# Optimization experiments

Hardware: AMD Instinct MI355X
Metric: run time of the kernel (lower is better)

The kernel has to match this reference:

```python
import jax, jax.numpy as jnp
import numpy as np

N_NODES = 100000
N_EDGES = 1600000
IN_FEATS = 128
HIDDEN = 128
NUM_CLASSES = 64


def setup_inputs() -> dict:
    key = jax.random.key(0)
    k1, k2, k3, k4, k5 = jax.random.split(key, 5)
    inputs = jax.random.normal(k1, (N_NODES, IN_FEATS), dtype=jnp.float32)
    src = jax.random.randint(k2, (N_EDGES,), 0, N_NODES, dtype=jnp.int32)
    dst = jax.random.randint(k3, (N_EDGES,), 0, N_NODES, dtype=jnp.int32)
    W1 = jax.random.normal(k4, (IN_FEATS, HIDDEN), dtype=jnp.float32) / np.sqrt(IN_FEATS)
    b1 = jnp.zeros((HIDDEN,), dtype=jnp.float32)
    W2 = jax.random.normal(k5, (HIDDEN, NUM_CLASSES), dtype=jnp.float32) / np.sqrt(HIDDEN)
    b2 = jnp.zeros((NUM_CLASSES,), dtype=jnp.float32)
    return {"inputs": inputs, "src": src, "dst": dst, "W1": W1, "b1": b1, "W2": W2, "b2": b2}


def _graph_conv(x, src, dst, W, b, n_nodes):
    # DGL GraphConv, norm='both': h = D_in^{-1/2} A D_out^{-1/2} x W + b
    ones = jnp.ones(src.shape[0], dtype=x.dtype)
    deg_out = jax.ops.segment_sum(ones, src, num_segments=n_nodes)
    deg_in = jax.ops.segment_sum(ones, dst, num_segments=n_nodes)
    norm_src = jax.lax.rsqrt(jnp.clip(deg_out, 1.0))  # [N]
    norm_dst = jax.lax.rsqrt(jnp.clip(deg_in, 1.0))   # [N]
    x = x * norm_src[:, None]
    msgs = x[src]                                      # [E, d] gather
    agg = jax.ops.segment_sum(msgs, dst, num_segments=n_nodes)  # [N, d] scatter-add
    agg = agg * norm_dst[:, None]
    return agg @ W + b


def reference(inputs, src, dst, W1, b1, W2, b2):
    n = inputs.shape[0]
    h = _graph_conv(inputs, src, dst, W1, b1, n)
    h = jax.nn.relu(h)
    h = _graph_conv(h, src, dst, W2, b2, n)
    return h
```

## Files before the change

### kernel.cpp

```cpp
#include <hip/hip_runtime.h>
#include <hip/hip_bf16.h>

#define N_FEATS_IN 128
#define BK_BITS 8
#define BK_SIZE 256
#define EPB 4096
#define MAXNB 512

typedef _Float16 h8 __attribute__((ext_vector_type(8)));
typedef float    f4v __attribute__((ext_vector_type(4)));
typedef float    f8v __attribute__((ext_vector_type(8)));

__device__ inline int wave_incl_scan(int v) {
    const int lane = threadIdx.x & 63;
    for (int off = 1; off < 64; off <<= 1) {
        int u = __shfl_up(v, off, 64);
        if (lane >= off) v += u;
    }
    return v;
}

__device__ inline int block_excl_scan(int s, int* ws, int* total) {
    const int lane = threadIdx.x & 63, wid = threadIdx.x >> 6;
    int inc = wave_incl_scan(s);
    if (lane == 63) ws[wid] = inc;
    __syncthreads();
    int woff = 0;
#pragma unroll
    for (int w = 0; w < 4; ++w) woff += (w < wid) ? ws[w] : 0;
    if (total) *total = ws[0] + ws[1] + ws[2] + ws[3];
    return woff + inc - s;
}

__global__ __launch_bounds__(256) void hist_kernel(
    const int* __restrict__ src, const int* __restrict__ dst,
    int* __restrict__ bh_d, int* __restrict__ bh_s,
    const float* __restrict__ W1, const float* __restrict__ W2,
    _Float16* __restrict__ wf1g, _Float16* __restrict__ wf2g,
    int E, int NB) {
    __shared__ int hd[MAXNB];
    __shared__ int hs[MAXNB];
    const int t = threadIdx.x;

    const int widx = blockIdx.x * 256 + t;
    if (widx < 128 * 128) {
        const int i = widx;
        const int k = i >> 7, c = i & 127;
        const int tt = c >> 4, s = k >> 5, q = (k >> 3) & 3, j = k & 7;
        wf1g[(((tt * 4 + s) * 4 + q) * 16 + (c & 15)) * 8 + j] =
            (_Float16)W1[i];
    } else if (widx < 128 * 128 + 128 * 64) {
        const int i = widx - 128 * 128;
        const int k = i >> 6, c = i & 63;
        const int tt = c >> 4, s = k >> 5, q = (k >> 3) & 3, j = k & 7;
        wf2g[(((tt * 4 + s) * 4 + q) * 16 + (c & 15)) * 8 + j] =
            (_Float16)W2[i];
    }

    for (int i = t; i < NB; i += 256) { hd[i] = 0; hs[i] = 0; }
    __syncthreads();
    const int base = blockIdx.x * EPB;
    const int end = min(base + EPB, E);
    for (int e = base + t; e < end; e += 256) {
        atomicAdd(&hd[dst[e] >> BK_BITS], 1);
        atomicAdd(&hs[src[e] >> BK_BITS], 1);
    }
    __syncthreads();
    for (int i = t; i < NB; i += 256) {
        bh_d[(size_t)blockIdx.x * NB + i] = hd[i];
        bh_s[(size_t)blockIdx.x * NB + i] = hs[i];
    }
}

__global__ __launch_bounds__(256) void colprefix2_kernel(
    int* __restrict__ bh_d, int* __restrict__ bh_s,
    int* __restrict__ tot_d, int* __restrict__ tot_s, int NBLK, int NB) {
    __shared__ int ws[4];
    const int b = blockIdx.x;
    const int t = threadIdx.x;
    int carry = 0;
    for (int base = 0; base < NBLK; base += 256) {
        const int r = base + t;
        const int v = (r < NBLK) ? bh_d[(size_t)r * NB + b] : 0;
        int total;
        const int e = block_excl_scan(v, ws, &total);
        if (r < NBLK) bh_d[(size_t)r * NB + b] = carry + e;
        carry += total;
        __syncthreads();
    }
    if (t == 0) tot_d[b] = carry;
    carry = 0;
    for (int base = 0; base < NBLK; base += 256) {
        const int r = base + t;
        const int v = (r < NBLK) ? bh_s[(size_t)r * NB + b] : 0;
        int total;
        const int e = block_excl_scan(v, ws, &total);
        if (r < NBLK) bh_s[(size_t)r * NB + b] = carry + e;
        carry += total;
        __syncthreads();
    }
    if (t == 0) tot_s[b] = carry;
}

__global__ __launch_bounds__(256) void bscan2_kernel(
    const int* __restrict__ tot_d, const int* __restrict__ tot_s,
    int* __restrict__ gb_d, int* __restrict__ gb_s,
    int* __restrict__ row_ptr, int NB, int N, int E) {
    __shared__ int ws[4];
    const int t = threadIdx.x;
    const int i0 = t * 4;
    {
        int a[4];
#pragma unroll
        for (int u = 0; u < 4; ++u) a[u] = (i0 + u < NB) ? tot_d[i0 + u] : 0;
        int e0 = block_excl_scan(a[0] + a[1] + a[2] + a[3], ws, nullptr);
#pragma unroll
        for (int u = 0; u < 4; ++u) {
            if (i0 + u < NB) gb_d[i0 + u] = e0;
            e0 += a[u];
        }
    }
    __syncthreads();
    {
        int a[4];
#pragma unroll
        for (int u = 0; u < 4; ++u) a[u] = (i0 + u < NB) ? tot_s[i0 + u] : 0;
        int e0 = block_excl_scan(a[0] + a[1] + a[2] + a[3], ws, nullptr);
#pragma unroll
        for (int u = 0; u < 4; ++u) {
            if (i0 + u < NB) gb_s[i0 + u] = e0;
            e0 += a[u];
        }
    }
    if (t == 0) { gb_d[NB] = E; gb_s[NB] = E; row_ptr[N] = E; }
}

__global__ __launch_bounds__(256) void scatter2_kernel(
    const int* __restrict__ src, const int* __restrict__ dst,
    const int* __restrict__ bh_d, const int* __restrict__ bh_s,
    const int* __restrict__ gb_d, const int* __restrict__ gb_s,
    unsigned int* __restrict__ ebuf, unsigned char* __restrict__ sbuf,
    int E, int NB) {
    __shared__ unsigned int eb_val[EPB];
    __shared__ int eb_dst[EPB];
    __shared__ int cur[MAXNB];
    __shared__ int bd[MAXNB];
    __shared__ int ws[4];
    const int t = threadIdx.x;
    const int base = blockIdx.x * EPB;
    const int end = min(base + EPB, E);
    const int tot = end - base;
    constexpr int ITER = EPB / 256;

    unsigned sv[ITER];
    int dv[ITER];
    for (int i = t; i < MAXNB; i += 256) cur[i] = 0;
    __syncthreads();
#pragma unroll
    for (int u = 0; u < ITER; ++u) {
        const int e = base + t + u * 256;
        if (e < end) {
            sv[u] = (unsigned)src[e];
            dv[u] = dst[e];
            atomicAdd(&cur[dv[u] >> BK_BITS], 1);
        } else {
            dv[u] = -1;
            sv[u] = 0;
        }
    }
    __syncthreads();

    {
        const int i0 = 2 * t, i1 = 2 * t + 1;
        const int a = cur[i0], b = cur[i1];
        const int e0 = block_excl_scan(a + b, ws, nullptr);
        const int g0 = (i0 < NB)
            ? gb_d[i0] + bh_d[(size_t)blockIdx.x * NB + i0] : 0;
        const int g1 = (i1 < NB)
            ? gb_d[i1] + bh_d[(size_t)blockIdx.x * NB + i1] : 0;
        cur[i0] = e0;
        cur[i1] = e0 + a;
        bd[i0] = g0 - e0;
        bd[i1] = g1 - (e0 + a);
    }
    __syncthreads();
#pragma unroll
    for (int u = 0; u < ITER; ++u) {
        if (dv[u] >= 0) {
            const int b = dv[u] >> BK_BITS;
            const int pos = atomicAdd(&cur[b], 1);
            eb_val[pos] = (sv[u] << 8) | (unsigned)(dv[u] & (BK_SIZE - 1));
            eb_dst[pos] = bd[b] + pos;
        }
    }
    __syncthreads();
    for (int i = t; i < tot; i += 256)
        ebuf[eb_dst[i]] = eb_val[i];
    __syncthreads();

    for (int i = t; i < MAXNB; i += 256) cur[i] = 0;
    __syncthreads();
#pragma unroll
    for (int u = 0; u < ITER; ++u)
        if (dv[u] >= 0) atomicAdd(&cur[(int)(sv[u] >> BK_BITS)], 1);
    __syncthreads();
    {
        const int i0 = 2 * t, i1 = 2 * t + 1;
        const int a = cur[i0], b = cur[i1];
        const int e0 = block_excl_scan(a + b, ws, nullptr);
        const int g0 = (i0 < NB)
            ? gb_s[i0] + bh_s[(size_t)blockIdx.x * NB + i0] : 0;
        const int g1 = (i1 < NB)
            ? gb_s[i1] + bh_s[(size_t)blockIdx.x * NB + i1] : 0;
        cur[i0] = e0;
        cur[i1] = e0 + a;
        bd[i0] = g0 - e0;
        bd[i1] = g1 - (e0 + a);
    }
    __syncthreads();
    unsigned char* sb_val = (unsigned char*)eb_val;
#pragma unroll
    for (int u = 0; u < ITER; ++u) {
        if (dv[u] >= 0) {
            const int b = (int)(sv[u] >> BK_BITS);
            const int pos = atomicAdd(&cur[b], 1);
            sb_val[pos] = (unsigned char)(sv[u] & (BK_SIZE - 1));
            eb_dst[pos] = bd[b] + pos;
        }
    }
    __syncthreads();
    for (int i = t; i < tot; i += 256)
        sbuf[eb_dst[i]] = sb_val[i];
}

__global__ __launch_bounds__(256) void bucket_csr_kernel(
    const unsigned int* __restrict__ ebuf, const int* __restrict__ gb_d,
    const unsigned char* __restrict__ sbuf, const int* __restrict__ gb_s,
    int* __restrict__ row_ptr, float* __restrict__ norm_dst,
    float* __restrict__ norm_src, int* __restrict__ edge_src, int N) {
    __shared__ int cnt[BK_SIZE];
    __shared__ int lro[BK_SIZE];
    __shared__ int ws[4];
    const int b = blockIdx.x;
    const int t = threadIdx.x;
    const int beg = gb_d[b], end = gb_d[b + 1];
    const int node = b * BK_SIZE + t;

    cnt[t] = 0;
    __syncthreads();
    for (int j = beg + t; j < end; j += 256)
        atomicAdd(&cnt[ebuf[j] & (BK_SIZE - 1)], 1);
    __syncthreads();

    const int v = cnt[t];
    const int excl = block_excl_scan(v, ws, nullptr);
    lro[t] = beg + excl;
    if (node < N) {
        row_ptr[node] = beg + excl;
        norm_dst[node] = rsqrtf(fmaxf((float)v, 1.0f));
    }
    __syncthreads();
    cnt[t] = 0;
    __syncthreads();

    for (int j = beg + t; j < end; j += 256) {
        const unsigned int ed = ebuf[j];
        const int dl = ed & (BK_SIZE - 1);
        const int p = atomicAdd(&cnt[dl], 1);
        edge_src[lro[dl] + p] = (int)(ed >> 8);
    }

    __syncthreads();
    cnt[t] = 0;
    __syncthreads();
    const int sb = gb_s[b], se = gb_s[b + 1];
    for (int j = sb + t; j < se; j += 256)
        atomicAdd(&cnt[sbuf[j]], 1);
    __syncthreads();
    if (node < N)
        norm_src[node] = rsqrtf(fmaxf((float)cnt[t], 1.0f));
}

template <int OC, bool XHALF>
__global__ __launch_bounds__(256) void mfma_gemm_kernel(
    const void* __restrict__ Xv, const _Float16* __restrict__ Wg,
    const float* __restrict__ scale, _Float16* __restrict__ Y, int n) {
    constexpr int K = 128;
    constexpr int NT = OC / 16;
    constexpr int RPB = 128;
    __shared__ _Float16 Wf[NT * 4 * 64 * 8];

    const int tid = threadIdx.x;
    for (int i = tid * 8; i < K * OC; i += 256 * 8)
        *(h8*)&Wf[i] = *(const h8*)&Wg[i];
    __syncthreads();

    const int lane = tid & 63;
    const int wv = tid >> 6;
    const int m = lane & 15, q = lane >> 4;

#pragma unroll
    for (int it = 0; it < RPB / 64; ++it) {
        const int rbase = blockIdx.x * RPB + it * 64 + wv * 16;
        const int lrow = min(rbase + m, n - 1);

        h8 a[4];
        if constexpr (XHALF) {
            const _Float16* X = (const _Float16*)Xv;
            const _Float16* p = &X[(size_t)lrow * K + q * 8];
#pragma unroll
            for (int s = 0; s < 4; ++s) a[s] = *(const h8*)(p + s * 32);
        } else {
            const float* X = (const float*)Xv;
            const float* p = &X[(size_t)lrow * K + q * 8];
#pragma unroll
            for (int s = 0; s < 4; ++s) {
                const float4 u0 = *(const float4*)(p + s * 32);
                const float4 u1 = *(const float4*)(p + s * 32 + 4);
                h8 v;
                v[0] = (_Float16)u0.x; v[1] = (_Float16)u0.y;
                v[2] = (_Float16)u0.z; v[3] = (_Float16)u0.w;
                v[4] = (_Float16)u1.x; v[5] = (_Float16)u1.y;
                v[6] = (_Float16)u1.z; v[7] = (_Float16)u1.w;
                a[s] = v;
            }
        }

        f4v acc[NT];
#pragma unroll
        for (int t = 0; t < NT; ++t) acc[t] = (f4v)0.0f;

#pragma unroll
        for (int s = 0; s < 4; ++s) {
#pragma unroll
            for (int t = 0; t < NT; ++t) {
                const h8 b = *(const h8*)&Wf[((t * 4 + s) * 64 + lane) * 8];
                acc[t] = __builtin_amdgcn_mfma_f32_16x16x32_f16(
                    a[s], b, acc[t], 0, 0, 0);
            }
        }

#pragma unroll
        for (int r = 0; r < 4; ++r) {
            const int orow = rbase + q * 4 + r;
            if (orow < n) {
                const float sc = scale[orow];
#pragma unroll
                for (int t = 0; t < NT; ++t)
                    Y[(size_t)orow * OC + t * 16 + m] =
                        (_Float16)(acc[t][r] * sc);
            }
        }
    }
}

template <int TPN>
__device__ inline f8v gather_rows(const h8* __restrict__ T8,
                                  const int* __restrict__ edge_src,
                                  int beg, int end, int f8) {
    f8v acc = (f8v)0.0f;
    int j = beg;
    for (; j + 15 < end; j += 16) {
        int s[16];
#pragma unroll
        for (int u = 0; u < 16; ++u) s[u] = edge_src[j + u];
        h8 a[16];
#pragma unroll
        for (int u = 0; u < 16; ++u) a[u] = T8[(size_t)s[u] * TPN + f8];
#pragma unroll
        for (int u = 0; u < 16; ++u)
            acc += __builtin_convertvector(a[u], f8v);
    }
    for (; j + 7 < end; j += 8) {
        int s[8];
#pragma unroll
        for (int u = 0; u < 8; ++u) s[u] = edge_src[j + u];
        h8 a[8];
#pragma unroll
        for (int u = 0; u < 8; ++u) a[u] = T8[(size_t)s[u] * TPN + f8];
#pragma unroll
        for (int u = 0; u < 8; ++u)
            acc += __builtin_convertvector(a[u], f8v);
    }
    for (; j + 3 < end; j += 4) {
        int s[4];
#pragma unroll
        for (int u = 0; u < 4; ++u) s[u] = edge_src[j + u];
        h8 a[4];
#pragma unroll
        for (int u = 0; u < 4; ++u) a[u] = T8[(size_t)s[u] * TPN + f8];
#pragma unroll
        for (int u = 0; u < 4; ++u)
            acc += __builtin_convertvector(a[u], f8v);
    }
    for (; j < end; ++j)
        acc += __builtin_convertvector(T8[(size_t)edge_src[j] * TPN + f8], f8v);
    return acc;
}

template <int FEAT, bool RELU, bool OUT_HALF>
__global__ __launch_bounds__(256) void gather_agg_kernel(
    const _Float16* __restrict__ T, const int* __restrict__ row_ptr,
    const int* __restrict__ edge_src, const float* __restrict__ norm_dst,
    const float* __restrict__ bias, void* __restrict__ outv, int n) {
    constexpr int TPN = FEAT / 8;
    constexpr int NPB = 256 / TPN;
    const int node = blockIdx.x * NPB + threadIdx.x / TPN;
    const int f8 = threadIdx.x % TPN;
    if (node >= n) return;
    const int beg = row_ptr[node];
    const int end = row_ptr[node + 1];

    f8v acc = gather_rows<TPN>((const h8*)T, edge_src, beg, end, f8);

    const float nd = norm_dst[node];
    float r[8];
#pragma unroll
    for (int k = 0; k < 8; ++k) {
        r[k] = acc[k] * nd + bias[f8 * 8 + k];
        if constexpr (RELU) r[k] = fmaxf(r[k], 0.0f);
    }

    if constexpr (OUT_HALF) {
        _Float16* out = (_Float16*)outv;
        h8 o;
#pragma unroll
        for (int k = 0; k < 8; ++k) o[k] = (_Float16)r[k];
        *(h8*)&out[(size_t)node * FEAT + f8 * 8] = o;
    } else {
        float* out = (float*)outv;
        float4 o0 = make_float4(r[0], r[1], r[2], r[3]);
        float4 o1 = make_float4(r[4], r[5], r[6], r[7]);
        *(float4*)&out[(size_t)node * FEAT + f8 * 8] = o0;
        *(float4*)&out[(size_t)node * FEAT + f8 * 8 + 4] = o1;
    }
}

template <int FEAT, int OC>
__global__ __launch_bounds__(256) void gather_gemm_kernel(
    const _Float16* __restrict__ T, const int* __restrict__ row_ptr,
    const int* __restrict__ edge_src, const float* __restrict__ norm_dst,
    const float* __restrict__ norm_src, const float* __restrict__ bias,
    const _Float16* __restrict__ Wg, _Float16* __restrict__ Y, int n) {
    constexpr int TPN = FEAT / 8;
    constexpr int NPB = 256 / TPN;
    constexpr int AP = FEAT + 8;
    __shared__ _Float16 Ah[NPB * AP];

    const int tid = threadIdx.x;
    const int node = blockIdx.x * NPB + tid / TPN;
    const int f8 = tid % TPN;
    const int nl = tid / TPN;

    float r[8];
    if (node < n) {
        const int beg = row_ptr[node];
        const int end = row_ptr[node + 1];
        f8v acc = gather_rows<TPN>((const h8*)T, edge_src, beg, end, f8);

        const float nd = norm_dst[node];
        const float ns = norm_src[node];
#pragma unroll
        for (int k = 0; k < 8; ++k) {
            float v = acc[k] * nd + bias[f8 * 8 + k];
            v = fmaxf(v, 0.0f);
            r[k] = v * ns;
        }
    } else {
#pragma unroll
        for (int k = 0; k < 8; ++k) r[k] = 0.0f;
    }

    {
        h8 av;
#pragma unroll
        for (int k = 0; k < 8; ++k) av[k] = (_Float16)r[k];
        *(h8*)&Ah[nl * AP + f8 * 8] = av;
    }
    __syncthreads();

    const int lane = tid & 63, w = tid >> 6;
    const int m = lane & 15, q = lane >> 4;
    f4v acc2 = (f4v)0.0f;
#pragma unroll
    for (int s = 0; s < 4; ++s) {
        const h8 a = *(const h8*)&Ah[m * AP + s * 32 + q * 8];
        const h8 b = *(const h8*)&Wg[((w * 4 + s) * 64 + lane) * 8];
        acc2 = __builtin_amdgcn_mfma_f32_16x16x32_f16(a, b, acc2, 0, 0, 0);
    }
#pragma unroll
    for (int rr = 0; rr < 4; ++rr) {
        const int orow = blockIdx.x * NPB + q * 4 + rr;
        if (orow < n)
            Y[(size_t)orow * OC + w * 16 + m] = (_Float16)acc2[rr];
    }
}

extern "C" void kernel_launch(void* const* d_in, const int* in_sizes, int n_in,
                              void* d_out, int out_size, void* d_ws, size_t ws_size,
                              hipStream_t stream) {
    const float* x   = (const float*)d_in[0];
    const int*   src = (const int*)d_in[1];
    const int*   dst = (const int*)d_in[2];
    const float* W1  = (const float*)d_in[3];
    const float* b1  = (const float*)d_in[4];
    const float* W2  = (const float*)d_in[5];
    const float* b2  = (const float*)d_in[6];
    float* out = (float*)d_out;

    const int N = in_sizes[0] / N_FEATS_IN;
    const int E = in_sizes[1];
    const int NB = (N + BK_SIZE - 1) / BK_SIZE;
    const int NBLK = (E + EPB - 1) / EPB;

    auto align4 = [](size_t w) { return (w + 3) & ~(size_t)3; };
    char* base = (char*)d_ws;
    size_t off = 0;
    auto take = [&](size_t words) {
        char* p = base + off * 4;
        off = align4(off + words);
        return p;
    };
    int*   tot_d    = (int*)take(NB);
    int*   tot_s    = (int*)take(NB);
    int*   gb_d     = (int*)take(NB + 1);
    int*   gb_s     = (int*)take(NB + 1);
    int*   bh_d     = (int*)take((size_t)NBLK * NB);
    int*   bh_s     = (int*)take((size_t)NBLK * NB);
    unsigned int*  ebuf = (unsigned int*)take(E);
    unsigned char* sbuf = (unsigned char*)take((E + 3) / 4);
    int*   row_ptr  = (int*)take(N + 1);
    int*   edge_src = (int*)take(E);
    float* norms    = (float*)take(2 * (size_t)N);
    _Float16* t1    = (_Float16*)take((size_t)N * 64);
    _Float16* t2    = (_Float16*)take((size_t)N * 32);
    _Float16* wf1g  = (_Float16*)take(128 * 128 / 2);
    _Float16* wf2g  = (_Float16*)take(128 * 64 / 2);
    float* norm_src = norms;
    float* norm_dst = norms + N;

    hist_kernel<<<NBLK, 256, 0, stream>>>(src, dst, bh_d, bh_s,
                                          W1, W2, wf1g, wf2g, E, NB);
    colprefix2_kernel<<<NB, 256, 0, stream>>>(bh_d, bh_s, tot_d, tot_s,
                                              NBLK, NB);
    bscan2_kernel<<<1, 256, 0, stream>>>(tot_d, tot_s, gb_d, gb_s, row_ptr,
                                         NB, N, E);
    scatter2_kernel<<<NBLK, 256, 0, stream>>>(src, dst, bh_d, bh_s, gb_d, gb_s,
                                              ebuf, sbuf, E, NB);
    bucket_csr_kernel<<<NB, 256, 0, stream>>>(ebuf, gb_d, sbuf, gb_s, row_ptr,
                                              norm_dst, norm_src, edge_src, N);

    mfma_gemm_kernel<128, false><<<(N + 127) / 128, 256, 0, stream>>>(
        x, wf1g, norm_src, t1, N);

    gather_gemm_kernel<128, 64><<<(N + 15) / 16, 256, 0, stream>>>(
        t1, row_ptr, edge_src, norm_dst, norm_src, b1, wf2g, t2, N);

    gather_agg_kernel<64, false, false><<<(N + 31) / 32, 256, 0, stream>>>(
        t2, row_ptr, edge_src, norm_dst, b2, out, N);
}
```

Before: 298.7 us.

## Replace per-block histogram prefix scan with global atomic bucket counters

Drops the per-block bucket histogram matrix and the column-prefix kernel. Block histograms are now summed into global bucket totals with atomics, and each scatter block claims its slice of a bucket through an atomicAdd on a running counter seeded from the bucket scan. This saves a kernel launch plus the NBLK×NB histogram writes and reads, but adds two memsets and global atomic contention. Edge order within a bucket becomes nondeterministic, which could change floating-point summation order downstream.

After: 331.7 us. 1.11x slower.

```diff
diff --git a/kernel.cpp b/kernel.cpp
--- a/kernel.cpp
+++ b/kernel.cpp
@@ -34,7 +34,7 @@
 
 __global__ __launch_bounds__(256) void hist_kernel(
     const int* __restrict__ src, const int* __restrict__ dst,
-    int* __restrict__ bh_d, int* __restrict__ bh_s,
+    int* __restrict__ tot_d, int* __restrict__ tot_s,
     const float* __restrict__ W1, const float* __restrict__ W2,
     _Float16* __restrict__ wf1g, _Float16* __restrict__ wf2g,
     int E, int NB) {
@@ -67,44 +67,16 @@
     }
     __syncthreads();
     for (int i = t; i < NB; i += 256) {
-        bh_d[(size_t)blockIdx.x * NB + i] = hd[i];
-        bh_s[(size_t)blockIdx.x * NB + i] = hs[i];
-    }
-}
-
-__global__ __launch_bounds__(256) void colprefix2_kernel(
-    int* __restrict__ bh_d, int* __restrict__ bh_s,
-    int* __restrict__ tot_d, int* __restrict__ tot_s, int NBLK, int NB) {
-    __shared__ int ws[4];
-    const int b = blockIdx.x;
-    const int t = threadIdx.x;
-    int carry = 0;
-    for (int base = 0; base < NBLK; base += 256) {
-        const int r = base + t;
-        const int v = (r < NBLK) ? bh_d[(size_t)r * NB + b] : 0;
-        int total;
-        const int e = block_excl_scan(v, ws, &total);
-        if (r < NBLK) bh_d[(size_t)r * NB + b] = carry + e;
-        carry += total;
-        __syncthreads();
-    }
-    if (t == 0) tot_d[b] = carry;
-    carry = 0;
-    for (int base = 0; base < NBLK; base += 256) {
-        const int r = base + t;
-        const int v = (r < NBLK) ? bh_s[(size_t)r * NB + b] : 0;
-        int total;
-        const int e = block_excl_scan(v, ws, &total);
-        if (r < NBLK) bh_s[(size_t)r * NB + b] = carry + e;
-        carry += total;
-        __syncthreads();
-    }
-    if (t == 0) tot_s[b] = carry;
+        const int a = hd[i], b = hs[i];
+        if (a) atomicAdd(&tot_d[i], a);
+        if (b) atomicAdd(&tot_s[i], b);
+    }
 }
 
 __global__ __launch_bounds__(256) void bscan2_kernel(
     const int* __restrict__ tot_d, const int* __restrict__ tot_s,
     int* __restrict__ gb_d, int* __restrict__ gb_s,
+    int* __restrict__ cnt_d, int* __restrict__ cnt_s,
     int* __restrict__ row_ptr, int NB, int N, int E) {
     __shared__ int ws[4];
     const int t = threadIdx.x;
@@ -116,7 +88,7 @@
         int e0 = block_excl_scan(a[0] + a[1] + a[2] + a[3], ws, nullptr);
 #pragma unroll
         for (int u = 0; u < 4; ++u) {
-            if (i0 + u < NB) gb_d[i0 + u] = e0;
+            if (i0 + u < NB) { gb_d[i0 + u] = e0; cnt_d[i0 + u] = e0; }
             e0 += a[u];
         }
     }
@@ -128,7 +100,7 @@
         int e0 = block_excl_scan(a[0] + a[1] + a[2] + a[3], ws, nullptr);
 #pragma unroll
         for (int u = 0; u < 4; ++u) {
-            if (i0 + u < NB) gb_s[i0 + u] = e0;
+            if (i0 + u < NB) { gb_s[i0 + u] = e0; cnt_s[i0 + u] = e0; }
             e0 += a[u];
         }
     }
@@ -137,8 +109,7 @@
 
 __global__ __launch_bounds__(256) void scatter2_kernel(
     const int* __restrict__ src, const int* __restrict__ dst,
-    const int* __restrict__ bh_d, const int* __restrict__ bh_s,
-    const int* __restrict__ gb_d, const int* __restrict__ gb_s,
+    int* __restrict__ cnt_d, int* __restrict__ cnt_s,
     unsigned int* __restrict__ ebuf, unsigned char* __restrict__ sbuf,
     int E, int NB) {
     __shared__ unsigned int eb_val[EPB];
@@ -174,10 +145,9 @@
         const int i0 = 2 * t, i1 = 2 * t + 1;
         const int a = cur[i0], b = cur[i1];
         const int e0 = block_excl_scan(a + b, ws, nullptr);
-        const int g0 = (i0 < NB)
-            ? gb_d[i0] + bh_d[(size_t)blockIdx.x * NB + i0] : 0;
-        const int g1 = (i1 < NB)
-            ? gb_d[i1] + bh_d[(size_t)blockIdx.x * NB + i1] : 0;
+        int g0 = 0, g1 = 0;
+        if (i0 < NB && a > 0) g0 = atomicAdd(&cnt_d[i0], a);
+        if (i1 < NB && b > 0) g1 = atomicAdd(&cnt_d[i1], b);
         cur[i0] = e0;
         cur[i1] = e0 + a;
         bd[i0] = g0 - e0;
@@ -208,10 +178,9 @@
         const int i0 = 2 * t, i1 = 2 * t + 1;
         const int a = cur[i0], b = cur[i1];
         const int e0 = block_excl_scan(a + b, ws, nullptr);
-        const int g0 = (i0 < NB)
-            ? gb_s[i0] + bh_s[(size_t)blockIdx.x * NB + i0] : 0;
-        const int g1 = (i1 < NB)
-            ? gb_s[i1] + bh_s[(size_t)blockIdx.x * NB + i1] : 0;
+        int g0 = 0, g1 = 0;
+        if (i0 < NB && a > 0) g0 = atomicAdd(&cnt_s[i0], a);
+        if (i1 < NB && b > 0) g1 = atomicAdd(&cnt_s[i1], b);
         cur[i0] = e0;
         cur[i1] = e0 + a;
         bd[i0] = g0 - e0;
@@ -525,8 +494,8 @@
     int*   tot_s    = (int*)take(NB);
     int*   gb_d     = (int*)take(NB + 1);
     int*   gb_s     = (int*)take(NB + 1);
-    int*   bh_d     = (int*)take((size_t)NBLK * NB);
-    int*   bh_s     = (int*)take((size_t)NBLK * NB);
+    int*   cnt_d    = (int*)take(NB);
+    int*   cnt_s    = (int*)take(NB);
     unsigned int*  ebuf = (unsigned int*)take(E);
     unsigned char* sbuf = (unsigned char*)take((E + 3) / 4);
     int*   row_ptr  = (int*)take(N + 1);
@@ -539,13 +508,13 @@
     float* norm_src = norms;
     float* norm_dst = norms + N;
 
-    hist_kernel<<<NBLK, 256, 0, stream>>>(src, dst, bh_d, bh_s,
+    hipMemsetAsync(tot_d, 0, (size_t)NB * sizeof(int), stream);
+    hipMemsetAsync(tot_s, 0, (size_t)NB * sizeof(int), stream);
+    hist_kernel<<<NBLK, 256, 0, stream>>>(src, dst, tot_d, tot_s,
                                           W1, W2, wf1g, wf2g, E, NB);
-    colprefix2_kernel<<<NB, 256, 0, stream>>>(bh_d, bh_s, tot_d, tot_s,
-                                              NBLK, NB);
-    bscan2_kernel<<<1, 256, 0, stream>>>(tot_d, tot_s, gb_d, gb_s, row_ptr,
-                                         NB, N, E);
-    scatter2_kernel<<<NBLK, 256, 0, stream>>>(src, dst, bh_d, bh_s, gb_d, gb_s,
+    bscan2_kernel<<<1, 256, 0, stream>>>(tot_d, tot_s, gb_d, gb_s,
+                                         cnt_d, cnt_s, row_ptr, NB, N, E);
+    scatter2_kernel<<<NBLK, 256, 0, stream>>>(src, dst, cnt_d, cnt_s,
                                               ebuf, sbuf, E, NB);
     bucket_csr_kernel<<<NB, 256, 0, stream>>>(ebuf, gb_d, sbuf, gb_s, row_ptr,
                                               norm_dst, norm_src, edge_src, N);
```
